# Kernel tuning notes

Hardware: AMD Instinct MI355X
Metric: run time of the kernel (lower is better)

## Reference

```python
import jax, jax.numpy as jnp
import numpy as np
import math

L, H, HD, D = 3, 8, 32, 256
TN, TE = 4, 3


def _layer_norm(x, g, b, eps=1e-5):
    m = jnp.mean(x, axis=-1, keepdims=True)
    v = jnp.var(x, axis=-1, keepdims=True)
    return (x - m) / jnp.sqrt(v + eps) * g + b


def _typed_transform(xh, W, types):
    # xh: [M, H, d], W: [T, H, d, d], types: [M] int -> per-row type-specific matmul
    out = jnp.zeros_like(xh)
    for t in range(W.shape[0]):
        y = jnp.einsum('mhd,hde->mhe', xh, W[t])
        out = jnp.where((types == t)[:, None, None], y, out)
    return out


def setup_inputs() -> dict:
    N, E = 20000, 320000
    key = jax.random.key(0)
    ks = jax.random.split(key, 16)
    inp = {}
    inp['x'] = jax.random.normal(ks[0], (N, D), dtype=jnp.float32)
    inp['edge_index'] = jax.random.randint(ks[1], (2, E), 0, N)
    inp['edge_type'] = jax.random.randint(ks[2], (E,), 0, TE)
    inp['node_type'] = jax.random.randint(ks[3], (N,), 0, TN)
    inp['W_Q'] = jax.random.normal(ks[4], (L, TN, H, HD, HD), dtype=jnp.float32) * 0.02
    inp['W_K'] = jax.random.normal(ks[5], (L, TN, H, HD, HD), dtype=jnp.float32) * 0.02
    inp['W_V'] = jax.random.normal(ks[6], (L, TN, H, HD, HD), dtype=jnp.float32) * 0.02
    inp['W_E'] = jax.random.normal(ks[7], (L, TE, H, HD, HD), dtype=jnp.float32) * 0.02
    inp['mu'] = jnp.ones((L, H, TE), dtype=jnp.float32)
    inp['Wo'] = jax.random.normal(ks[8], (L, D, D), dtype=jnp.float32) * 0.02
    inp['bo'] = jnp.zeros((L, D), dtype=jnp.float32)
    inp['ln1_g'] = jnp.ones((L, D), dtype=jnp.float32)
    inp['ln1_b'] = jnp.zeros((L, D), dtype=jnp.float32)
    inp['ln2_g'] = jnp.ones((L, D), dtype=jnp.float32)
    inp['ln2_b'] = jnp.zeros((L, D), dtype=jnp.float32)
    inp['w1'] = jax.random.normal(ks[9], (L, D, 4 * D), dtype=jnp.float32) * 0.02
    inp['b1'] = jnp.zeros((L, 4 * D), dtype=jnp.float32)
    inp['w2'] = jax.random.normal(ks[10], (L, 4 * D, D), dtype=jnp.float32) * 0.02
    inp['b2'] = jnp.zeros((L, D), dtype=jnp.float32)
    inp['out_g'] = jnp.ones((D,), dtype=jnp.float32)
    inp['out_b'] = jnp.zeros((D,), dtype=jnp.float32)
    return inp


def reference(x, edge_index, edge_type, node_type, W_Q, W_K, W_V, W_E, mu,
              Wo, bo, ln1_g, ln1_b, ln2_g, ln2_b, w1, b1, w2, b2, out_g, out_b):
    N = x.shape[0]
    src, dst = edge_index[0], edge_index[1]
    scale = math.sqrt(HD)
    for l in range(L):
        xh = x.reshape(N, H, HD)
        Q = _typed_transform(xh, W_Q[l], node_type)
        K = _typed_transform(xh, W_K[l], node_type)
        V = _typed_transform(xh, W_V[l], node_type)
        q_dst = Q[dst]                                  # [E,H,hd]
        kt = _typed_transform(K[src], W_E[l], edge_type)  # per-edge-type transform
        scores = jnp.sum(q_dst * kt, axis=-1) / scale   # [E,H]
        scores = scores * mu[l].T[edge_type]            # mu[l]: [H,TE] -> [E,H]
        m = jax.ops.segment_max(scores, dst, num_segments=N)
        m = jnp.maximum(m, -1e9)                        # match torch -1e9 init
        e = jnp.exp(scores - m[dst])
        s = jax.ops.segment_sum(e, dst, num_segments=N)
        w = e / (s[dst] + 1e-10)
        agg = jax.ops.segment_sum(V[src] * w[..., None], dst, num_segments=N)
        attn = agg.reshape(N, D) @ Wo[l] + bo[l]
        x = _layer_norm(x + attn, ln1_g[l], ln1_b[l])
        h = jax.nn.gelu(x @ w1[l] + b1[l], approximate=False) @ w2[l] + b2[l]
        x = _layer_norm(x + h, ln2_g[l], ln2_b[l])
    return _layer_norm(x, out_g, out_b)
```

## Files before the change

### kernel.cpp

```cpp
#include <hip/hip_runtime.h>
#include <hip/hip_fp8.h>
#include <math.h>

#define HDIM 32
#define NHEAD 8
#define DMODEL 256
#define NTYPE 4
#define ETYPE 3
#define NLAYER 3

typedef unsigned short u16;
typedef unsigned char u8;
typedef __bf16 bf16x8 __attribute__((ext_vector_type(8)));
typedef float f32x4 __attribute__((ext_vector_type(4)));

__device__ __forceinline__ u16 f2bf(float f) {
  union { float f; unsigned u; } v; v.f = f;
  unsigned r = v.u + 0x7FFF + ((v.u >> 16) & 1);
  return (u16)(r >> 16);
}
__device__ __forceinline__ float bf2f(u16 b) {
  union { unsigned u; float f; } v; v.u = (unsigned)b << 16; return v.f;
}
__device__ __forceinline__ u8 f2fp8(float v) {
  __hip_fp8_e4m3 t(v); return (u8)t.__x;
}
__device__ __forceinline__ float fp82f(unsigned b) {
  __hip_fp8_e4m3 t; t.__x = (__hip_fp8_storage_t)b; return (float)t;
}

__device__ __forceinline__ float gelu_f(float v) {
  float u = 0.7978845608028654f * v * (1.f + 0.044715f * v * v);
  float e = __expf(-2.f * fabsf(u));
  float th = (1.f - e) / (1.f + e);
  th = copysignf(th, u);
  return 0.5f * v * (1.f + th);
}

#define GLDS16(g, l)                                              \
  __builtin_amdgcn_global_load_lds(                               \
      (const __attribute__((address_space(1))) void*)(g),         \
      (__attribute__((address_space(3))) void*)(l), 16, 0, 0)

__global__ void count_deg_kernel(const int* __restrict__ dst, int* __restrict__ deg, int E) {
  int tid = blockIdx.x * 256 + threadIdx.x;
  if (tid < E) atomicAdd(&deg[dst[tid]], 1);
}

__global__ __launch_bounds__(1024) void scan_kernel(const int* __restrict__ deg,
                                                    int* __restrict__ off, int n) {
  __shared__ int part[1024];
  int t = threadIdx.x;
  int chunk = (n + 1023) >> 10;
  int base = t * chunk;
  int s = 0;
  for (int i = 0; i < chunk; ++i) {
    int idx = base + i;
    if (idx < n) s += deg[idx];
  }
  part[t] = s;
  __syncthreads();
  for (int o = 1; o < 1024; o <<= 1) {
    int v = (t >= o) ? part[t - o] : 0;
    __syncthreads();
    part[t] += v;
    __syncthreads();
  }
  int run = part[t] - s;
  for (int i = 0; i < chunk; ++i) {
    int idx = base + i;
    if (idx < n) { off[idx] = run; run += deg[idx]; }
  }
  if (t == 1023) off[n] = part[1023];
}

__global__ void scatter_kernel(const int* __restrict__ src, const int* __restrict__ dst,
                               const int* __restrict__ etype,
                               const int* __restrict__ off, int* __restrict__ cursor,
                               int* __restrict__ csr_src, int* __restrict__ csr_dst,
                               int* __restrict__ csr_et, int E) {
  int tid = blockIdx.x * 256 + threadIdx.x;
  if (tid < E) {
    int d = dst[tid];
    int p = atomicAdd(&cursor[d], 1);
    int pos = off[d] + p;
    csr_src[pos] = src[tid];
    csr_dst[pos] = d;
    csr_et[pos] = etype[tid];
  }
}

__global__ void tcount_kernel(const int* __restrict__ nt, int* __restrict__ tcnt, int N) {
  __shared__ int h[NTYPE];
  int t = threadIdx.x;
  if (t < NTYPE) h[t] = 0;
  __syncthreads();
  int tid = blockIdx.x * 256 + t;
  if (tid < N) atomicAdd(&h[nt[tid]], 1);
  __syncthreads();
  if (t < NTYPE && h[t] > 0) atomicAdd(&tcnt[t], h[t]);
}

__global__ void tscan_kernel(const int* __restrict__ tcnt, int* __restrict__ toff,
                             int* __restrict__ tile_off) {
  if (threadIdx.x == 0 && blockIdx.x == 0) {
    int o = 0, to = 0;
    for (int t = 0; t < NTYPE; ++t) {
      toff[t] = o; tile_off[t] = to;
      o += tcnt[t]; to += (tcnt[t] + 63) >> 6;
    }
    toff[NTYPE] = o; tile_off[NTYPE] = to;
  }
}

__global__ void tscatter_kernel(const int* __restrict__ nt, const int* __restrict__ toff,
                                int* __restrict__ tcur, int* __restrict__ tidx, int N) {
  int tid = blockIdx.x * 256 + threadIdx.x;
  int lane = threadIdx.x & 63;
  int ty = (tid < N) ? nt[tid] : -1;
  unsigned long long lt_mask = (lane == 63) ? 0x7FFFFFFFFFFFFFFFull
                                            : ((1ull << lane) - 1);
#pragma unroll
  for (int t4 = 0; t4 < NTYPE; ++t4) {
    unsigned long long mask = __ballot(ty == t4);
    if (mask == 0) continue;
    int first = __builtin_ctzll(mask);
    int cnt = __popcll(mask);
    int base = 0;
    if (lane == first) base = atomicAdd(&tcur[t4], cnt);
    base = __shfl(base, first, 64);
    if (ty == t4) {
      int rank = __popcll(mask & lt_mask);
      tidx[toff[t4] + base + rank] = tid;
    }
  }
}

__global__ void xconv_kernel(const float* __restrict__ x, u16* __restrict__ xb, int n4) {
  int i = blockIdx.x * 256 + threadIdx.x;
  if (i < n4) {
    float4 v = ((const float4*)x)[i];
    ushort4 o = { f2bf(v.x), f2bf(v.y), f2bf(v.z), f2bf(v.w) };
    ((ushort4*)xb)[i] = o;
  }
}

__global__ __launch_bounds__(256) void wprep_kernel(
    const float* __restrict__ W_Q, const float* __restrict__ W_K,
    const float* __restrict__ W_V, const float* __restrict__ W_E,
    u16* __restrict__ wqkvb) {
  int b = blockIdx.x;
  int h = b & 7, tt = (b >> 3) & 3, l = b >> 5;
  __shared__ float wq[1024];
  __shared__ float we[3][1024];
  int t = threadIdx.x;
  const float* WQp = W_Q + (((size_t)l * NTYPE + tt) * NHEAD + h) * 1024;
  for (int i = t; i < 1024; i += 256) wq[i] = WQp[i];
  for (int et = 0; et < ETYPE; ++et) {
    const float* WEp = W_E + (((size_t)l * ETYPE + et) * NHEAD + h) * 1024;
    for (int i = t; i < 1024; i += 256) we[et][i] = WEp[i];
  }
  __syncthreads();
  const float* WKp = W_K + (((size_t)l * NTYPE + tt) * NHEAD + h) * 1024;
  const float* WVp = W_V + (((size_t)l * NTYPE + tt) * NHEAD + h) * 1024;
  u16* out = wqkvb + (size_t)b * 5120;
  for (int i = t; i < 1024; i += 256) {
    int col = i >> 5, k = i & 31;
    out[i] = f2bf(WKp[k * 32 + col]);
    out[1024 + i] = f2bf(WVp[k * 32 + col]);
#pragma unroll
    for (int et = 0; et < ETYPE; ++et) {
      float a = 0.f;
#pragma unroll
      for (int j = 0; j < 32; ++j) a += wq[k * 32 + j] * we[et][col * 32 + j];
      out[(2 + et) * 1024 + i] = f2bf(a);
    }
  }
}

__global__ __launch_bounds__(256) void qkv_mfma(
    const u16* __restrict__ xb, const int* __restrict__ tidx,
    const int* __restrict__ toff, const int* __restrict__ tile_off,
    const u16* __restrict__ wqkvb_l,
    u8* __restrict__ Kb8, u8* __restrict__ Vb8, u16* __restrict__ Qeb) {
  __shared__ u16 smem[10240];
  int bx = blockIdx.x, h = blockIdx.y;
  if (bx >= tile_off[NTYPE]) return;
  int ty = 0;
  while (bx >= tile_off[ty + 1]) ++ty;
  int lt = bx - tile_off[ty];
  int base = toff[ty] + lt * 64;
  int cnt = min(64, toff[ty + 1] - toff[ty] - lt * 64);
  int t = threadIdx.x;
  {
    int row = ((t >> 6) << 4) | (t & 15);
    int q = (t >> 4) & 3;
    int node = tidx[base + min(row, cnt - 1)];
    *(uint4*)&smem[t * 8] =
        *(const uint4*)&xb[(size_t)node * 256 + h * 32 + q * 8];
  }
  const u16* wsrc = wqkvb_l + ((size_t)ty * NHEAD + h) * 5120;
  for (int dc = t; dc < 640; dc += 256) {
    int mt = dc >> 7, wi = dc & 127, slot = wi >> 5, colx = wi & 31;
    *(uint4*)&smem[2048 + dc * 8] = *(const uint4*)&wsrc[(mt * 128 + colx * 4 + slot) * 8];
  }
  __syncthreads();

  int lane = t & 63, w = t >> 6;
  int m = lane & 15, q = lane >> 4;
  bf16x8 af = *(const bf16x8*)&smem[w * 512 + q * 128 + m * 8];
  f32x4 acc[5][2];
#pragma unroll
  for (int mt = 0; mt < 5; ++mt)
#pragma unroll
    for (int c = 0; c < 2; ++c) {
      bf16x8 bf = *(const bf16x8*)&smem[2048 + mt * 1024 + q * 256 + (c * 16 + m) * 8];
      acc[mt][c] = __builtin_amdgcn_mfma_f32_16x16x32_bf16(af, bf, (f32x4){0.f, 0.f, 0.f, 0.f}, 0, 0, 0);
    }
  __syncthreads();
#pragma unroll
  for (int mt = 0; mt < 5; ++mt)
#pragma unroll
    for (int c = 0; c < 2; ++c)
#pragma unroll
      for (int r = 0; r < 4; ++r)
        smem[mt * 2048 + (w * 16 + q * 4 + r) * 32 + c * 16 + m] = f2bf(acc[mt][c][r]);
  __syncthreads();
  {
    int row = t >> 2, q4 = t & 3;
    if (row < cnt) {
      int node = tidx[base + row];
      {
        const u16* sp = &smem[row * 32 + q4 * 8];
        unsigned long long pk = 0;
#pragma unroll
        for (int j = 0; j < 8; ++j)
          pk |= (unsigned long long)f2fp8(bf2f(sp[j])) << (8 * j);
        *(unsigned long long*)&Kb8[(size_t)node * 256 + h * 32 + q4 * 8] = pk;
      }
      {
        const u16* sp = &smem[2048 + row * 32 + q4 * 8];
        unsigned long long pk = 0;
#pragma unroll
        for (int j = 0; j < 8; ++j)
          pk |= (unsigned long long)f2fp8(bf2f(sp[j])) << (8 * j);
        *(unsigned long long*)&Vb8[(size_t)node * 256 + h * 32 + q4 * 8] = pk;
      }
#pragma unroll
      for (int et = 0; et < ETYPE; ++et)
        *(uint4*)&Qeb[((size_t)node * ETYPE + et) * 256 + h * 32 + q4 * 8] =
            *(const uint4*)&smem[(2 + et) * 2048 + row * 32 + q4 * 8];
    }
  }
}

__global__ __launch_bounds__(256) void score_kernel(
    const int* __restrict__ csr_src, const int* __restrict__ csr_dst,
    const int* __restrict__ csr_et, const u16* __restrict__ Qeb,
    const u8* __restrict__ Kb8, const float* __restrict__ mu,
    float* __restrict__ scores, int E) {
  int tid = blockIdx.x * 256 + threadIdx.x;
  if (tid >= E * NHEAD) return;
  int p = tid >> 3, h = tid & 7;
  int s = csr_src[p], d = csr_dst[p], t = csr_et[p];
  const bf16x8* q = (const bf16x8*)(Qeb + ((size_t)d * ETYPE + t) * 256 + h * 32);
  const uint2* k = (const uint2*)(Kb8 + (size_t)s * 256 + h * 32);
  float acc = 0.f;
#pragma unroll
  for (int g = 0; g < 4; ++g) {
    uint2 kd = k[g];
    bf16x8 qq = q[g];
#pragma unroll
    for (int b = 0; b < 4; ++b) {
      acc += fp82f((kd.x >> (8 * b)) & 0xffu) * (float)qq[b];
      acc += fp82f((kd.y >> (8 * b)) & 0xffu) * (float)qq[4 + b];
    }
  }
  scores[tid] = __expf(acc * 0.17677669529663687f * mu[h * ETYPE + t]);
}

__global__ __launch_bounds__(256) void agg_kernel(
    const int* __restrict__ off, const int* __restrict__ csr_src,
    const float* __restrict__ scores, const u8* __restrict__ Vb8,
    u16* __restrict__ aggb) {
  __shared__ float sacc[4][256];
  __shared__ float sssum[4][8];
  int n = blockIdx.x;
  int t = threadIdx.x;
  int g = t >> 6;
  int l = t & 63;
  int d0 = l * 4;
  int h = l >> 3;
  int s0 = off[n], s1 = off[n + 1];
  float a0 = 0.f, a1 = 0.f, a2 = 0.f, a3 = 0.f, ssum = 0.f;
  for (int k = s0 + g; k < s1; k += 4) {
    int sn = csr_src[k];
    float e = scores[(size_t)k * 8 + h];
    unsigned v4 = *(const unsigned*)(Vb8 + (size_t)sn * 256 + d0);
    a0 += e * fp82f(v4 & 0xffu);
    a1 += e * fp82f((v4 >> 8) & 0xffu);
    a2 += e * fp82f((v4 >> 16) & 0xffu);
    a3 += e * fp82f((v4 >> 24) & 0xffu);
    ssum += e;
  }
  *(float4*)&sacc[g][d0] = make_float4(a0, a1, a2, a3);
  if ((l & 7) == 0) sssum[g][h] = ssum;
  __syncthreads();
  int hh = t >> 5;
  float tot = sacc[0][t] + sacc[1][t] + sacc[2][t] + sacc[3][t];
  float st = sssum[0][hh] + sssum[1][hh] + sssum[2][hh] + sssum[3][hh];
  aggb[(size_t)n * 256 + t] = f2bf(tot / (st + 1e-10f));
}

__global__ __launch_bounds__(256) void convT_kernel(const float* __restrict__ W,
                                                    u16* __restrict__ Wt, int K, int Nc) {
  __shared__ float tile[32][33];
  int bk = blockIdx.y * 32, bn = blockIdx.x * 32;
  const float* Wz = W + (size_t)blockIdx.z * K * Nc;
  u16* Wtz = Wt + (size_t)blockIdx.z * K * Nc;
  int tx = threadIdx.x & 31, ty = threadIdx.x >> 5;
  for (int r = ty; r < 32; r += 8)
    tile[r][tx] = Wz[(size_t)(bk + r) * Nc + bn + tx];
  __syncthreads();
  for (int r = ty; r < 32; r += 8)
    Wtz[(size_t)(bn + r) * K + bk + tx] = f2bf(tile[tx][r]);
}

template <int GELU, int BN>
__global__ __launch_bounds__(256) void gemm_mfma(
    const u16* __restrict__ A, const u16* __restrict__ Bt,
    const float* __restrict__ bias, u16* __restrict__ Cb,
    int M, int K, int Nc) {
  constexpr int MJ = BN / 32;
  __shared__ u16 As[128 * 32];
  __shared__ u16 Bs[BN * 32];
  const int t = threadIdx.x;
  const int lane = t & 63;
  const int w = t >> 6;
  const int row0 = blockIdx.y * 128;
  const int col0 = blockIdx.x * BN;
  const int wm = (w >> 1) * 64, wn = (w & 1) * (BN / 2);

  f32x4 acc[4][MJ] = {};
  const int sr = lane >> 2;
  const int sk0 = lane & 3;
  const int sks = sk0 ^ ((sr >> 1) & 3);

  for (int k0 = 0; k0 < K; k0 += 32) {
#pragma unroll
    for (int c = 0; c < 2; ++c) {
      const int chunk = w * 2 + c;
      const int r = chunk * 16 + sr;
      int ra = row0 + r; if (ra >= M) ra = M - 1;
      GLDS16(A + (size_t)ra * K + k0 + sks * 8, &As[(chunk * 64 + lane) * 8]);
      if (BN == 128) {
        GLDS16(Bt + (size_t)(col0 + r) * K + k0 + sks * 8, &Bs[(chunk * 64 + lane) * 8]);
      }
    }
    if (BN == 64) {
      const int r = w * 16 + sr;
      GLDS16(Bt + (size_t)(col0 + r) * K + k0 + sks * 8, &Bs[(w * 64 + lane) * 8]);
    }
    __syncthreads();
    bf16x8 af[4], bfr[MJ];
    const int ks = lane >> 4;
    const int lr = lane & 15;
    const int rsl = ks ^ ((lr >> 1) & 3);
#pragma unroll
    for (int i = 0; i < 4; ++i)
      af[i] = *(const bf16x8*)&As[(((wm >> 4) + i) * 64 + lr * 4 + rsl) * 8];
#pragma unroll
    for (int j = 0; j < MJ; ++j)
      bfr[j] = *(const bf16x8*)&Bs[(((wn >> 4) + j) * 64 + lr * 4 + rsl) * 8];
#pragma unroll
    for (int i = 0; i < 4; ++i)
#pragma unroll
      for (int j = 0; j < MJ; ++j)
        acc[i][j] = __builtin_amdgcn_mfma_f32_16x16x32_bf16(af[i], bfr[j], acc[i][j], 0, 0, 0);
    __syncthreads();
  }

  const int lc = lane & 15;
  const int lrow = (lane >> 4) * 4;
  float bv[MJ];
#pragma unroll
  for (int j = 0; j < MJ; ++j) bv[j] = bias[col0 + wn + j * 16 + lc];
#pragma unroll
  for (int i = 0; i < 4; ++i) {
#pragma unroll
    for (int r = 0; r < 4; ++r) {
      int gr = row0 + wm + i * 16 + lrow + r;
      if (gr >= M) continue;
#pragma unroll
      for (int j = 0; j < MJ; ++j) {
        int gc = col0 + wn + j * 16 + lc;
        float v = acc[i][j][r] + bv[j];
        if (GELU) v = gelu_f(v);
        Cb[(size_t)gr * Nc + gc] = f2bf(v);
      }
    }
  }
}

__global__ __launch_bounds__(256) void ln_kernel(
    const float* __restrict__ xin, const u16* __restrict__ res,
    const float* __restrict__ g, const float* __restrict__ b,
    float* __restrict__ out, u16* __restrict__ outb, int N) {
  int row = blockIdx.x * 4 + (threadIdx.x >> 6);
  if (row >= N) return;
  int l = threadIdx.x & 63;
  size_t base = (size_t)row * 256 + l * 4;
  float4 r4 = *(const float4*)&xin[base];
  if (res) {
    ushort4 rb = *(const ushort4*)&res[base];
    r4.x += bf2f(rb.x); r4.y += bf2f(rb.y);
    r4.z += bf2f(rb.z); r4.w += bf2f(rb.w);
  }
  float s = r4.x + r4.y + r4.z + r4.w;
  for (int o = 32; o > 0; o >>= 1) s += __shfl_xor(s, o, 64);
  float m = s * (1.f / 256.f);
  float dx = r4.x - m, dy = r4.y - m, dz = r4.z - m, dw = r4.w - m;
  float s2 = dx * dx + dy * dy + dz * dz + dw * dw;
  for (int o = 32; o > 0; o >>= 1) s2 += __shfl_xor(s2, o, 64);
  float inv = rsqrtf(s2 * (1.f / 256.f) + 1e-5f);
  float4 g4 = *(const float4*)&g[l * 4];
  float4 b4 = *(const float4*)&b[l * 4];
  float4 o4 = { dx * inv * g4.x + b4.x, dy * inv * g4.y + b4.y,
                dz * inv * g4.z + b4.z, dw * inv * g4.w + b4.w };
  *(float4*)&out[base] = o4;
  if (outb) {
    ushort4 ob = { f2bf(o4.x), f2bf(o4.y), f2bf(o4.z), f2bf(o4.w) };
    *(ushort4*)&outb[base] = ob;
  }
}

extern "C" void kernel_launch(void* const* d_in, const int* in_sizes, int n_in,
                              void* d_out, int out_size, void* d_ws, size_t ws_size,
                              hipStream_t stream) {
  const float* x_in   = (const float*)d_in[0];
  const int*   ei     = (const int*)d_in[1];
  const int*   etype  = (const int*)d_in[2];
  const int*   ntype  = (const int*)d_in[3];
  const float* W_Q    = (const float*)d_in[4];
  const float* W_K    = (const float*)d_in[5];
  const float* W_V    = (const float*)d_in[6];
  const float* W_E    = (const float*)d_in[7];
  const float* mu     = (const float*)d_in[8];
  const float* Wo     = (const float*)d_in[9];
  const float* bo     = (const float*)d_in[10];
  const float* ln1g   = (const float*)d_in[11];
  const float* ln1b   = (const float*)d_in[12];
  const float* ln2g   = (const float*)d_in[13];
  const float* ln2b   = (const float*)d_in[14];
  const float* w1     = (const float*)d_in[15];
  const float* b1     = (const float*)d_in[16];
  const float* w2     = (const float*)d_in[17];
  const float* b2     = (const float*)d_in[18];
  const float* outg   = (const float*)d_in[19];
  const float* outb   = (const float*)d_in[20];

  const int N = in_sizes[0] / DMODEL;
  const int E = in_sizes[1] / 2;
  const int* src = ei;
  const int* dst = ei + E;

  const size_t NF = (size_t)N * DMODEL;
  const size_t EH = (size_t)E * NHEAD;

  float* f      = (float*)d_ws;
  float* xbuf   = f;
  float* scores = f + NF;
  u16*   fout   = (u16*)(f + NF + EH);
  u16*   xb     = fout + NF;
  u16*   Qeb    = xb + NF;
  u16*   h1b    = Qeb;
  u16*   aggb   = Qeb + 3 * NF;
  u8*    Kb8    = (u8*)(aggb + NF);
  u8*    Vb8    = Kb8 + NF;
  u16*   wqkvb  = (u16*)(Vb8 + NF);
  u16*   Wot    = wqkvb + (size_t)NLAYER * NTYPE * NHEAD * 5120;
  u16*   w1t    = Wot + 3 * 65536;
  u16*   w2t    = w1t + 3 * 262144;
  int*   ip     = (int*)(w2t + 3 * 262144);
  int*   off    = ip;
  int*   csr_src= off + (N + 1);
  int*   csr_dst= csr_src + E;
  int*   csr_et = csr_dst + E;
  int*   cursor = csr_et + E;
  int*   tidx   = cursor + N;
  int*   toff   = tidx + N;
  int*   tile_off = toff + (NTYPE + 1);
  int*   tcnt   = tile_off + (NTYPE + 1);
  int*   tcur   = tcnt + NTYPE;

  hipMemsetAsync(cursor, 0, (size_t)N * sizeof(int), stream);
  hipMemsetAsync(tcnt, 0, 2 * NTYPE * sizeof(int), stream);
  count_deg_kernel<<<(E + 255) / 256, 256, 0, stream>>>(dst, cursor, E);
  scan_kernel<<<1, 1024, 0, stream>>>(cursor, off, N);
  hipMemsetAsync(cursor, 0, (size_t)N * sizeof(int), stream);
  scatter_kernel<<<(E + 255) / 256, 256, 0, stream>>>(
      src, dst, etype, off, cursor, csr_src, csr_dst, csr_et, E);
  tcount_kernel<<<(N + 255) / 256, 256, 0, stream>>>(ntype, tcnt, N);
  tscan_kernel<<<1, 64, 0, stream>>>(tcnt, toff, tile_off);
  tscatter_kernel<<<(N + 255) / 256, 256, 0, stream>>>(ntype, toff, tcur, tidx, N);

  wprep_kernel<<<NLAYER * NTYPE * NHEAD, 256, 0, stream>>>(W_Q, W_K, W_V, W_E, wqkvb);
  convT_kernel<<<dim3(DMODEL / 32, DMODEL / 32, NLAYER), 256, 0, stream>>>(
      Wo, Wot, DMODEL, DMODEL);
  convT_kernel<<<dim3(4 * DMODEL / 32, DMODEL / 32, NLAYER), 256, 0, stream>>>(
      w1, w1t, DMODEL, 4 * DMODEL);
  convT_kernel<<<dim3(DMODEL / 32, 4 * DMODEL / 32, NLAYER), 256, 0, stream>>>(
      w2, w2t, 4 * DMODEL, DMODEL);

  hipMemcpyAsync(xbuf, x_in, NF * sizeof(float), hipMemcpyDeviceToDevice, stream);
  xconv_kernel<<<(int)((NF / 4 + 255) / 256), 256, 0, stream>>>(x_in, xb, (int)(NF / 4));

  const int gm = (N + 127) / 128;
  const int lng = (N + 3) / 4;
  const int qtiles = (N + 63) / 64 + NTYPE;
  for (int l = 0; l < NLAYER; ++l) {
    qkv_mfma<<<dim3(qtiles, NHEAD), 256, 0, stream>>>(
        xb, tidx, toff, tile_off,
        wqkvb + (size_t)l * NTYPE * NHEAD * 5120, Kb8, Vb8, Qeb);
    score_kernel<<<(int)((EH + 255) / 256), 256, 0, stream>>>(
        csr_src, csr_dst, csr_et, Qeb, Kb8, mu + (size_t)l * NHEAD * ETYPE, scores, E);
    agg_kernel<<<N, 256, 0, stream>>>(off, csr_src, scores, Vb8, aggb);

    gemm_mfma<0, 64><<<dim3(DMODEL / 64, gm), 256, 0, stream>>>(
        aggb, Wot + (size_t)l * 65536, bo + (size_t)l * DMODEL,
        fout, N, DMODEL, DMODEL);
    ln_kernel<<<lng, 256, 0, stream>>>(xbuf, fout,
        ln1g + (size_t)l * DMODEL, ln1b + (size_t)l * DMODEL, xbuf, xb, N);
    gemm_mfma<1, 128><<<dim3(4 * DMODEL / 128, gm), 256, 0, stream>>>(
        xb, w1t + (size_t)l * 262144, b1 + (size_t)l * 4 * DMODEL,
        h1b, N, DMODEL, 4 * DMODEL);
    gemm_mfma<0, 64><<<dim3(DMODEL / 64, gm), 256, 0, stream>>>(
        h1b, w2t + (size_t)l * 262144, b2 + (size_t)l * DMODEL,
        fout, N, 4 * DMODEL, DMODEL);
    ln_kernel<<<lng, 256, 0, stream>>>(xbuf, fout,
        ln2g + (size_t)l * DMODEL, ln2b + (size_t)l * DMODEL, xbuf, xb, N);
  }

  ln_kernel<<<lng, 256, 0, stream>>>(xbuf, nullptr, outg, outb, (float*)d_out, nullptr, N);
}
```

Baseline: 796.7 us.

## Double K-step per barrier in MFMA GEMM and remap workgroups across XCDs

The bf16 MFMA GEMM now loads a 64-wide K slice per iteration (two 32-wide halves) into doubled shared buffers, which halves the number of barrier pairs per tile. It also drops the XOR swizzle on the shared-memory layout and remaps linear workgroup IDs so that consecutive tiles land on the same XCD, aiming for better L2 reuse. Removing the swizzle may reintroduce LDS bank conflicts on the fragment reads, and the doubled LDS footprint can lower occupancy. The code assumes K is a multiple of 64.

Result: faster. 756.0 us (-5.1%).

```diff
diff --git a/kernel.cpp b/kernel.cpp
--- a/kernel.cpp
+++ b/kernel.cpp
@@ -332,51 +332,67 @@
     const float* __restrict__ bias, u16* __restrict__ Cb,
     int M, int K, int Nc) {
   constexpr int MJ = BN / 32;
-  __shared__ u16 As[128 * 32];
-  __shared__ u16 Bs[BN * 32];
+  __shared__ u16 As[128 * 64];
+  __shared__ u16 Bs[BN * 64];
   const int t = threadIdx.x;
   const int lane = t & 63;
   const int w = t >> 6;
-  const int row0 = blockIdx.y * 128;
-  const int col0 = blockIdx.x * BN;
+
+  const int nwg = gridDim.x * gridDim.y;
+  const int lin = blockIdx.y * gridDim.x + blockIdx.x;
+  const int qq = nwg >> 3, rr = nwg & 7;
+  const int xcd = lin & 7, pos = lin >> 3;
+  const int nl = (xcd < rr ? xcd * (qq + 1) : rr * (qq + 1) + (xcd - rr) * qq) + pos;
+  const int row0 = (nl / gridDim.x) * 128;
+  const int col0 = (nl % gridDim.x) * BN;
+
   const int wm = (w >> 1) * 64, wn = (w & 1) * (BN / 2);
 
   f32x4 acc[4][MJ] = {};
   const int sr = lane >> 2;
-  const int sk0 = lane & 3;
-  const int sks = sk0 ^ ((sr >> 1) & 3);
-
-  for (int k0 = 0; k0 < K; k0 += 32) {
-#pragma unroll
-    for (int c = 0; c < 2; ++c) {
-      const int chunk = w * 2 + c;
-      const int r = chunk * 16 + sr;
-      int ra = row0 + r; if (ra >= M) ra = M - 1;
-      GLDS16(A + (size_t)ra * K + k0 + sks * 8, &As[(chunk * 64 + lane) * 8]);
-      if (BN == 128) {
-        GLDS16(Bt + (size_t)(col0 + r) * K + k0 + sks * 8, &Bs[(chunk * 64 + lane) * 8]);
+  const int sk = (lane & 3) * 8;
+
+  for (int k0 = 0; k0 < K; k0 += 64) {
+#pragma unroll
+    for (int half = 0; half < 2; ++half) {
+#pragma unroll
+      for (int c = 0; c < 2; ++c) {
+        const int chunk = w * 2 + c;
+        const int r = chunk * 16 + sr;
+        int ra = row0 + r; if (ra >= M) ra = M - 1;
+        GLDS16(A + (size_t)ra * K + k0 + half * 32 + sk,
+               &As[((half * 8 + chunk) * 64 + lane) * 8]);
+        if (BN == 128) {
+          GLDS16(Bt + (size_t)(col0 + r) * K + k0 + half * 32 + sk,
+                 &Bs[((half * 8 + chunk) * 64 + lane) * 8]);
+        }
       }
-    }
-    if (BN == 64) {
-      const int r = w * 16 + sr;
-      GLDS16(Bt + (size_t)(col0 + r) * K + k0 + sks * 8, &Bs[(w * 64 + lane) * 8]);
+      if (BN == 64) {
+        const int r = w * 16 + sr;
+        GLDS16(Bt + (size_t)(col0 + r) * K + k0 + half * 32 + sk,
+               &Bs[((half * 4 + w) * 64 + lane) * 8]);
+      }
     }
     __syncthreads();
-    bf16x8 af[4], bfr[MJ];
-    const int ks = lane >> 4;
+    const int ko = (lane >> 4) * 8;
     const int lr = lane & 15;
-    const int rsl = ks ^ ((lr >> 1) & 3);
-#pragma unroll
-    for (int i = 0; i < 4; ++i)
-      af[i] = *(const bf16x8*)&As[(((wm >> 4) + i) * 64 + lr * 4 + rsl) * 8];
-#pragma unroll
-    for (int j = 0; j < MJ; ++j)
-      bfr[j] = *(const bf16x8*)&Bs[(((wn >> 4) + j) * 64 + lr * 4 + rsl) * 8];
-#pragma unroll
-    for (int i = 0; i < 4; ++i)
+#pragma unroll
+    for (int half = 0; half < 2; ++half) {
+      bf16x8 af[4], bfr[MJ];
+      const int ab = half * 8 * 512;
+      const int bb = half * (BN == 128 ? 8 : 4) * 512;
+#pragma unroll
+      for (int i = 0; i < 4; ++i)
+        af[i] = *(const bf16x8*)&As[ab + ((wm >> 4) + i) * 512 + lr * 32 + ko];
 #pragma unroll
       for (int j = 0; j < MJ; ++j)
-        acc[i][j] = __builtin_amdgcn_mfma_f32_16x16x32_bf16(af[i], bfr[j], acc[i][j], 0, 0, 0);
+        bfr[j] = *(const bf16x8*)&Bs[bb + ((wn >> 4) + j) * 512 + lr * 32 + ko];
+#pragma unroll
+      for (int i = 0; i < 4; ++i)
+#pragma unroll
+        for (int j = 0; j < MJ; ++j)
+          acc[i][j] = __builtin_amdgcn_mfma_f32_16x16x32_bf16(af[i], bfr[j], acc[i][j], 0, 0, 0);
+    }
     __syncthreads();
   }
 
```
